# Performance work log

Measured on AMD Instinct MI355X. Metric: run time of the kernel, lower is better.

Reference implementation:

```python
import jax, jax.numpy as jnp
import numpy as np
import math

W_BITS = 256.0  # default w_bits in forward()

def ste_round(x):
    # straight-through estimator round: identity gradient
    return x + jax.lax.stop_gradient(jnp.round(x) - x)

def setup_inputs() -> dict:
    key = jax.random.key(0)
    k1, k2 = jax.random.split(key)
    x_size, y_size = 4096, 4096
    xb = jax.random.normal(k1, (8192, x_size), dtype=jnp.float32)
    W = jax.random.normal(k2, (x_size, y_size), dtype=jnp.float32) / math.sqrt(x_size)
    b = jnp.zeros((y_size,), dtype=jnp.float32)
    return {"xb": xb, "W": W, "b": b}

def reference(xb, W, b):
    # train=True path: fake-quant the weights (per-tensor symmetric int8), then matmul + bias
    s_w = 2.0 * jnp.max(jnp.abs(W)) / W_BITS          # per-tensor scale (zero-point 0)
    w_q = jnp.clip(ste_round(W / s_w), -127.0, 127.0)  # quantize + clamp
    w_fq = s_w * w_q                                    # dequantize (fake-quant)
    return xb @ w_fq + b
```

## Files before the change

### kernel.cpp

```cpp
#include <hip/hip_runtime.h>
#include <hip/hip_bf16.h>
#include <stdint.h>

typedef unsigned short u16;
typedef unsigned int u32;
typedef __bf16 bf16x8 __attribute__((ext_vector_type(8)));
typedef float f32x4 __attribute__((ext_vector_type(4)));
typedef u16 u16x4 __attribute__((ext_vector_type(4)));

typedef const __attribute__((address_space(1))) void* gas_ptr;
typedef __attribute__((address_space(3))) void* las_ptr;

#define M_DIM 8192
#define K_DIM 4096
#define N_DIM 4096

__device__ __forceinline__ u16 f32_to_bf16_rne(float f) {
    u32 u = __float_as_uint(f);
    u += 0x7FFFu + ((u >> 16) & 1u);
    return (u16)(u >> 16);
}

__global__ void maxabs_kernel(const float* __restrict__ W, u32* __restrict__ out, int n4) {
    int idx = blockIdx.x * blockDim.x + threadIdx.x;
    int stride = gridDim.x * blockDim.x;
    const float4* W4 = (const float4*)W;
    float m = 0.0f;
    for (int i = idx; i < n4; i += stride) {
        float4 v = W4[i];
        m = fmaxf(m, fmaxf(fmaxf(fabsf(v.x), fabsf(v.y)), fmaxf(fabsf(v.z), fabsf(v.w))));
    }
#pragma unroll
    for (int off = 32; off > 0; off >>= 1)
        m = fmaxf(m, __shfl_down(m, off));
    if ((threadIdx.x & 63) == 0)
        atomicMax(out, __float_as_uint(m));
}

__global__ void quant_transpose_kernel(const float* __restrict__ W, u16* __restrict__ Wt,
                                       const u32* __restrict__ mb) {
    __shared__ u16 tile[32][33];
    const float s_inv = 128.0f / __uint_as_float(*mb);
    int n = blockIdx.x * 32 + threadIdx.x;
#pragma unroll
    for (int r = threadIdx.y; r < 32; r += 8) {
        int k = blockIdx.y * 32 + r;
        float q = rintf(W[(size_t)k * N_DIM + n] * s_inv);
        q = fminf(fmaxf(q, -127.0f), 127.0f);
        tile[threadIdx.x][r] = (u16)(__float_as_uint(q) >> 16);
    }
    __syncthreads();
    int k_out = blockIdx.y * 32 + threadIdx.x;
#pragma unroll
    for (int r = threadIdx.y; r < 32; r += 8) {
        int n_out = blockIdx.x * 32 + r;
        Wt[(size_t)n_out * K_DIM + k_out] = tile[r][threadIdx.x];
    }
}

__global__ void cast_bf16_kernel(const float* __restrict__ x, u16* __restrict__ y, int n4) {
    int idx = blockIdx.x * blockDim.x + threadIdx.x;
    int stride = gridDim.x * blockDim.x;
    const float4* x4 = (const float4*)x;
    u16x4* y4 = (u16x4*)y;
    for (int i = idx; i < n4; i += stride) {
        float4 v = x4[i];
        u16x4 o;
        o.x = f32_to_bf16_rne(v.x);
        o.y = f32_to_bf16_rne(v.y);
        o.z = f32_to_bf16_rne(v.z);
        o.w = f32_to_bf16_rne(v.w);
        y4[i] = o;
    }
}

__global__ __launch_bounds__(256) void gemm_kernel(const u16* __restrict__ A,
                                                   const u16* __restrict__ Bt,
                                                   const float* __restrict__ bias,
                                                   const u32* __restrict__ mb,
                                                   float* __restrict__ out) {
    __shared__ u16 As[128 * 32];
    __shared__ u16 Bs[128 * 32];

    const int tid = threadIdx.x;
    const int wave = tid >> 6;
    const int lane = tid & 63;
    const int m0 = blockIdx.y * 128;
    const int n0 = blockIdx.x * 128;

    const int lrow = lane >> 2;
    const int lcol = (lane & 3) * 8;

    const u16* Ag0 = A + (size_t)(m0 + wave * 16 + lrow) * K_DIM + lcol;
    const u16* Ag1 = A + (size_t)(m0 + (wave + 4) * 16 + lrow) * K_DIM + lcol;
    const u16* Bg0 = Bt + (size_t)(n0 + wave * 16 + lrow) * K_DIM + lcol;
    const u16* Bg1 = Bt + (size_t)(n0 + (wave + 4) * 16 + lrow) * K_DIM + lcol;

    u16* Asl0 = &As[wave * 512];
    u16* Asl1 = &As[(wave + 4) * 512];
    u16* Bsl0 = &Bs[wave * 512];
    u16* Bsl1 = &Bs[(wave + 4) * 512];

    const int quad = lane >> 4;
    const int l15 = lane & 15;
    const int wm = wave >> 1;
    const int wn = wave & 1;

    const float s_w = __uint_as_float(*mb) * (1.0f / 128.0f);

    f32x4 acc[4][4];
#pragma unroll
    for (int i = 0; i < 4; i++)
#pragma unroll
        for (int j = 0; j < 4; j++) acc[i][j] = (f32x4){0.f, 0.f, 0.f, 0.f};

    for (int k0 = 0; k0 < K_DIM; k0 += 32) {
        __syncthreads();
        __builtin_amdgcn_global_load_lds((gas_ptr)(Ag0 + k0), (las_ptr)Asl0, 16, 0, 0);
        __builtin_amdgcn_global_load_lds((gas_ptr)(Ag1 + k0), (las_ptr)Asl1, 16, 0, 0);
        __builtin_amdgcn_global_load_lds((gas_ptr)(Bg0 + k0), (las_ptr)Bsl0, 16, 0, 0);
        __builtin_amdgcn_global_load_lds((gas_ptr)(Bg1 + k0), (las_ptr)Bsl1, 16, 0, 0);
        __syncthreads();

        bf16x8 af[4], bfr[4];
#pragma unroll
        for (int i = 0; i < 4; i++)
            af[i] = *(const bf16x8*)&As[(wm * 64 + i * 16 + l15) * 32 + quad * 8];
#pragma unroll
        for (int j = 0; j < 4; j++)
            bfr[j] = *(const bf16x8*)&Bs[(wn * 64 + j * 16 + l15) * 32 + quad * 8];

#pragma unroll
        for (int i = 0; i < 4; i++)
#pragma unroll
            for (int j = 0; j < 4; j++)
                acc[i][j] = __builtin_amdgcn_mfma_f32_16x16x32_bf16(af[i], bfr[j], acc[i][j], 0, 0, 0);
    }

#pragma unroll
    for (int j = 0; j < 4; j++) {
        const int col = n0 + wn * 64 + j * 16 + l15;
        const float bv = bias[col];
#pragma unroll
        for (int i = 0; i < 4; i++) {
            const int row = m0 + wm * 64 + i * 16 + quad * 4;
            float* op = out + (size_t)row * N_DIM + col;
#pragma unroll
            for (int r = 0; r < 4; r++) op[(size_t)r * N_DIM] = s_w * acc[i][j][r] + bv;
        }
    }
}

extern "C" void kernel_launch(void* const* d_in, const int* in_sizes, int n_in,
                              void* d_out, int out_size, void* d_ws, size_t ws_size,
                              hipStream_t stream) {
    const float* xb = (const float*)d_in[0];
    const float* W = (const float*)d_in[1];
    const float* b = (const float*)d_in[2];
    float* out = (float*)d_out;

    u32* mb = (u32*)d_ws;
    u16* xb_bf = (u16*)((char*)d_ws + 256);
    u16* wqt = (u16*)((char*)d_ws + 256 + (size_t)M_DIM * K_DIM * 2);

    hipMemsetAsync(d_ws, 0, 4, stream);
    maxabs_kernel<<<1024, 256, 0, stream>>>(W, mb, (K_DIM * N_DIM) / 4);
    quant_transpose_kernel<<<dim3(N_DIM / 32, K_DIM / 32), dim3(32, 8), 0, stream>>>(W, wqt, mb);
    cast_bf16_kernel<<<4096, 256, 0, stream>>>(xb, xb_bf, (M_DIM * K_DIM) / 4);
    gemm_kernel<<<dim3(N_DIM / 128, M_DIM / 128), 256, 0, stream>>>(xb_bf, wqt, b, mb, out);
}
```

Measured before the change: 635.1 us.

## Rewrite GEMM as 256x256 double-buffered, swizzled, 8-wave pipelined MFMA kernel

```diff
diff --git a/kernel.cpp b/kernel.cpp
--- a/kernel.cpp
+++ b/kernel.cpp
@@ -74,79 +74,227 @@
     }
 }
 
-__global__ __launch_bounds__(256) void gemm_kernel(const u16* __restrict__ A,
-                                                   const u16* __restrict__ Bt,
-                                                   const float* __restrict__ bias,
-                                                   const u32* __restrict__ mb,
-                                                   float* __restrict__ out) {
-    __shared__ u16 As[128 * 32];
-    __shared__ u16 Bs[128 * 32];
+
+#define BAR() __builtin_amdgcn_s_barrier()
+#define LGKM0()                                            \
+    do {                                                   \
+        asm volatile("s_waitcnt lgkmcnt(0)" ::: "memory"); \
+        __builtin_amdgcn_sched_barrier(0);                 \
+    } while (0)
+#define VMC(N) asm volatile("s_waitcnt vmcnt(" #N ")" ::: "memory")
+#define PRIO1() __builtin_amdgcn_s_setprio(1)
+#define PRIO0() __builtin_amdgcn_s_setprio(0)
+
+#define DS_A(ABASE, MH)                                            \
+    do {                                                           \
+        _Pragma("unroll") for (int i_ = 0; i_ < 4; ++i_) {         \
+            const char* p_ = (ABASE) + ((MH)*64 + i_ * 16) * 128;  \
+            a[i_][0] = *(const bf16x8*)(p_ + ck0);                 \
+            a[i_][1] = *(const bf16x8*)(p_ + ck1);                 \
+        }                                                          \
+    } while (0)
+
+#define DS_B(BBASE, NH)                                            \
+    do {                                                           \
+        _Pragma("unroll") for (int j_ = 0; j_ < 2; ++j_) {         \
+            const char* p_ = (BBASE) + ((NH)*32 + j_ * 16) * 128;  \
+            b[(NH)*2 + j_][0] = *(const bf16x8*)(p_ + ck0);        \
+            b[(NH)*2 + j_][1] = *(const bf16x8*)(p_ + ck1);        \
+        }                                                          \
+    } while (0)
+
+#define MM(MH, NH)                                                                            \
+    do {                                                                                      \
+        _Pragma("unroll") for (int i_ = 0; i_ < 4; ++i_) {                                    \
+            _Pragma("unroll") for (int j_ = 0; j_ < 2; ++j_) {                                \
+                f32x4& c_ = acc[(MH)*4 + i_][(NH)*2 + j_];                                    \
+                c_ = __builtin_amdgcn_mfma_f32_16x16x32_bf16(a[i_][0], b[(NH)*2 + j_][0], c_, \
+                                                             0, 0, 0);                        \
+                c_ = __builtin_amdgcn_mfma_f32_16x16x32_bf16(a[i_][1], b[(NH)*2 + j_][1], c_, \
+                                                             0, 0, 0);                        \
+            }                                                                                 \
+        }                                                                                     \
+    } while (0)
+
+#define STAGE_A(BUF, T, HALF)                                                                 \
+    do {                                                                                      \
+        const int r0_ = wave * 8 + (HALF)*64;                                                 \
+        const u16* s_ = Ag + (size_t)r0_ * K_DIM + (T)*64;                                    \
+        __builtin_amdgcn_global_load_lds((gas_ptr)s_, (las_ptr)&lds[BUF][r0_ * 64], 16, 0,    \
+                                         0);                                                  \
+        __builtin_amdgcn_global_load_lds((gas_ptr)(s_ + (size_t)128 * K_DIM),                 \
+                                         (las_ptr)&lds[BUF][(r0_ + 128) * 64], 16, 0, 0);     \
+    } while (0)
+
+#define STAGE_B(BUF, T, HALF)                                                                  \
+    do {                                                                                       \
+        const int r0_ = bw + (HALF)*32;                                                        \
+        const u16* s_ = Bg + (size_t)r0_ * K_DIM + (T)*64;                                     \
+        __builtin_amdgcn_global_load_lds((gas_ptr)s_, (las_ptr)&lds[2 + (BUF)][r0_ * 64], 16,  \
+                                         0, 0);                                                \
+        __builtin_amdgcn_global_load_lds((gas_ptr)(s_ + (size_t)128 * K_DIM),                  \
+                                         (las_ptr)&lds[2 + (BUF)][(r0_ + 128) * 64], 16, 0,    \
+                                         0);                                                   \
+    } while (0)
+
+#define TILE(ABASE, BBASE, BUF, PBUF, T)            \
+    do {                                            \
+        DS_A(ABASE, 0);                             \
+        DS_B(BBASE, 0);                             \
+        STAGE_A(PBUF, (T) + 1, 1);                  \
+        BAR();                                      \
+        LGKM0();                                    \
+        PRIO1();                                    \
+        MM(0, 0);                                   \
+        PRIO0();                                    \
+        BAR();                                      \
+        DS_B(BBASE, 1);                             \
+        STAGE_B(PBUF, (T) + 1, 1);                  \
+        BAR();                                      \
+        LGKM0();                                    \
+        PRIO1();                                    \
+        MM(0, 1);                                   \
+        PRIO0();                                    \
+        BAR();                                      \
+        DS_A(ABASE, 1);                             \
+        STAGE_A(BUF, (T) + 2, 0);                   \
+        BAR();                                      \
+        LGKM0();                                    \
+        PRIO1();                                    \
+        MM(1, 0);                                   \
+        PRIO0();                                    \
+        BAR();                                      \
+        STAGE_B(BUF, (T) + 2, 0);                   \
+        BAR();                                      \
+        PRIO1();                                    \
+        MM(1, 1);                                   \
+        PRIO0();                                    \
+        VMC(4);                                     \
+        BAR();                                      \
+    } while (0)
+
+__global__ __launch_bounds__(512, 2) void gemm_kernel(const u16* __restrict__ A,
+                                                      const u16* __restrict__ Bt,
+                                                      const float* __restrict__ bias,
+                                                      const u32* __restrict__ mb,
+                                                      float* __restrict__ out) {
+    extern __shared__ u16 lds_raw[];
+    u16(*lds)[256 * 64] = reinterpret_cast<u16(*)[256 * 64]>(lds_raw);
 
     const int tid = threadIdx.x;
     const int wave = tid >> 6;
     const int lane = tid & 63;
-    const int m0 = blockIdx.y * 128;
-    const int n0 = blockIdx.x * 128;
-
-    const int lrow = lane >> 2;
-    const int lcol = (lane & 3) * 8;
-
-    const u16* Ag0 = A + (size_t)(m0 + wave * 16 + lrow) * K_DIM + lcol;
-    const u16* Ag1 = A + (size_t)(m0 + (wave + 4) * 16 + lrow) * K_DIM + lcol;
-    const u16* Bg0 = Bt + (size_t)(n0 + wave * 16 + lrow) * K_DIM + lcol;
-    const u16* Bg1 = Bt + (size_t)(n0 + (wave + 4) * 16 + lrow) * K_DIM + lcol;
-
-    u16* Asl0 = &As[wave * 512];
-    u16* Asl1 = &As[(wave + 4) * 512];
-    u16* Bsl0 = &Bs[wave * 512];
-    u16* Bsl1 = &Bs[(wave + 4) * 512];
-
     const int quad = lane >> 4;
     const int l15 = lane & 15;
-    const int wm = wave >> 1;
-    const int wn = wave & 1;
+    const int wm = wave >> 2;
+    const int wn = wave & 3;
+
+    const int bswz = (blockIdx.x & 7) * 64 + (blockIdx.x >> 3);
+    const int m0 = (bswz >> 4) * 256;
+    const int n0 = (bswz & 15) * 256;
+
+    const int stg_row = lane >> 3;
+    const int stg_col = ((lane & 7) ^ stg_row) * 8;
+    const u16* Ag = A + (size_t)(m0 + stg_row) * K_DIM + stg_col;
+    const u16* Bg = Bt + (size_t)(n0 + stg_row) * K_DIM + stg_col;
+    const int bw = (wave & 3) * 8 + (wave >> 2) * 64;
+
+    const int xorv = (l15 & 7) << 4;
+    const int ck0 = (quad * 16) ^ xorv;
+    const int ck1 = (64 + quad * 16) ^ xorv;
+
+    const char* asb0 = (const char*)&lds[0][0] + wm * 16384 + l15 * 128;
+    const char* asb1 = asb0 + 32768;
+    const char* bsb0 = (const char*)&lds[2][0] + wn * 8192 + l15 * 128;
+    const char* bsb1 = bsb0 + 32768;
+
+    bf16x8 a[4][2];
+    bf16x8 b[4][2];
+    f32x4 acc[8][4];
+#pragma unroll
+    for (int i = 0; i < 8; i++)
+#pragma unroll
+        for (int j = 0; j < 4; j++) acc[i][j] = (f32x4){0.f, 0.f, 0.f, 0.f};
+
+    STAGE_A(0, 0, 0);
+    STAGE_A(0, 0, 1);
+    STAGE_B(0, 0, 0);
+    STAGE_B(0, 0, 1);
+    STAGE_A(1, 1, 0);
+    STAGE_B(1, 1, 0);
+    VMC(4);
+    BAR();
+
+#pragma unroll 1
+    for (int t = 0; t < 62; t += 2) {
+        TILE(asb0, bsb0, 0, 1, t);
+        TILE(asb1, bsb1, 1, 0, t + 1);
+    }
+
+    DS_A(asb0, 0);
+    DS_B(bsb0, 0);
+    STAGE_A(1, 63, 1);
+    BAR();
+    LGKM0();
+    PRIO1();
+    MM(0, 0);
+    PRIO0();
+    BAR();
+    DS_B(bsb0, 1);
+    STAGE_B(1, 63, 1);
+    BAR();
+    LGKM0();
+    PRIO1();
+    MM(0, 1);
+    PRIO0();
+    BAR();
+    DS_A(asb0, 1);
+    BAR();
+    LGKM0();
+    PRIO1();
+    MM(1, 0);
+    PRIO0();
+    BAR();
+    PRIO1();
+    MM(1, 1);
+    PRIO0();
+    VMC(0);
+    BAR();
+
+    DS_A(asb1, 0);
+    DS_B(bsb1, 0);
+    BAR();
+    LGKM0();
+    PRIO1();
+    MM(0, 0);
+    PRIO0();
+    BAR();
+    DS_B(bsb1, 1);
+    BAR();
+    LGKM0();
+    PRIO1();
+    MM(0, 1);
+    PRIO0();
+    BAR();
+    DS_A(asb1, 1);
+    BAR();
+    LGKM0();
+    PRIO1();
+    MM(1, 0);
+    MM(1, 1);
+    PRIO0();
 
     const float s_w = __uint_as_float(*mb) * (1.0f / 128.0f);
-
-    f32x4 acc[4][4];
-#pragma unroll
-    for (int i = 0; i < 4; i++)
-#pragma unroll
-        for (int j = 0; j < 4; j++) acc[i][j] = (f32x4){0.f, 0.f, 0.f, 0.f};
-
-    for (int k0 = 0; k0 < K_DIM; k0 += 32) {
-        __syncthreads();
-        __builtin_amdgcn_global_load_lds((gas_ptr)(Ag0 + k0), (las_ptr)Asl0, 16, 0, 0);
-        __builtin_amdgcn_global_load_lds((gas_ptr)(Ag1 + k0), (las_ptr)Asl1, 16, 0, 0);
-        __builtin_amdgcn_global_load_lds((gas_ptr)(Bg0 + k0), (las_ptr)Bsl0, 16, 0, 0);
-        __builtin_amdgcn_global_load_lds((gas_ptr)(Bg1 + k0), (las_ptr)Bsl1, 16, 0, 0);
-        __syncthreads();
-
-        bf16x8 af[4], bfr[4];
-#pragma unroll
-        for (int i = 0; i < 4; i++)
-            af[i] = *(const bf16x8*)&As[(wm * 64 + i * 16 + l15) * 32 + quad * 8];
-#pragma unroll
-        for (int j = 0; j < 4; j++)
-            bfr[j] = *(const bf16x8*)&Bs[(wn * 64 + j * 16 + l15) * 32 + quad * 8];
-
-#pragma unroll
-        for (int i = 0; i < 4; i++)
-#pragma unroll
-            for (int j = 0; j < 4; j++)
-                acc[i][j] = __builtin_amdgcn_mfma_f32_16x16x32_bf16(af[i], bfr[j], acc[i][j], 0, 0, 0);
-    }
-
-#pragma unroll
-    for (int j = 0; j < 4; j++) {
-        const int col = n0 + wn * 64 + j * 16 + l15;
+#pragma unroll
+    for (int nj = 0; nj < 4; ++nj) {
+        const int col = n0 + wn * 64 + nj * 16 + l15;
         const float bv = bias[col];
 #pragma unroll
-        for (int i = 0; i < 4; i++) {
-            const int row = m0 + wm * 64 + i * 16 + quad * 4;
+        for (int mi = 0; mi < 8; ++mi) {
+            const int row = m0 + wm * 128 + mi * 16 + quad * 4;
             float* op = out + (size_t)row * N_DIM + col;
 #pragma unroll
-            for (int r = 0; r < 4; r++) op[(size_t)r * N_DIM] = s_w * acc[i][j][r] + bv;
+            for (int r = 0; r < 4; ++r) op[(size_t)r * N_DIM] = s_w * acc[mi][nj][r] + bv;
         }
     }
 }
@@ -167,5 +315,5 @@
     maxabs_kernel<<<1024, 256, 0, stream>>>(W, mb, (K_DIM * N_DIM) / 4);
     quant_transpose_kernel<<<dim3(N_DIM / 32, K_DIM / 32), dim3(32, 8), 0, stream>>>(W, wqt, mb);
     cast_bf16_kernel<<<4096, 256, 0, stream>>>(xb, xb_bf, (M_DIM * K_DIM) / 4);
-    gemm_kernel<<<dim3(N_DIM / 128, M_DIM / 128), 256, 0, stream>>>(xb_bf, wqt, b, mb, out);
-}
+    gemm_kernel<<<dim3(512), dim3(512), 131072, stream>>>(xb_bf, wqt, b, mb, out);
+}
```

Result: faster. 535.7 us (-15.7%).
